# Kernel optimization log

Hardware: AMD Instinct MI355X
Metric: run time of the kernel (lower is better)

## Reference

```python
import jax, jax.numpy as jnp
import numpy as np

B, S, D, H, E = 8, 196, 768, 12, 8
HD = D // H  # 64
FF = 4 * D   # 3072
EPS = 1e-5


def setup_inputs() -> dict:
    key = jax.random.key(0)
    ks = jax.random.split(key, 12)
    s = 0.02
    inp = {
        'x': jax.random.normal(ks[0], (B, S, D), jnp.float32),
        'ln1_g': jnp.ones((D,), jnp.float32),
        'ln1_b': jnp.zeros((D,), jnp.float32),
        'Wq': jax.random.normal(ks[1], (D, D), jnp.float32) * s,
        'bq': jnp.zeros((D,), jnp.float32),
        'Wk': jax.random.normal(ks[2], (D, HD), jnp.float32) * s,
        'bk': jnp.zeros((HD,), jnp.float32),
        'Wv': jax.random.normal(ks[3], (D, HD), jnp.float32) * s,
        'bv': jnp.zeros((HD,), jnp.float32),
        'ln2_g': jnp.ones((D,), jnp.float32),
        'ln2_b': jnp.zeros((D,), jnp.float32),
        'Wg': jax.random.normal(ks[4], (D, E), jnp.float32) * s,
        'bg': jnp.zeros((E,), jnp.float32),
        'W1': jax.random.normal(ks[5], (E, D, FF), jnp.float32) * s,
        'b1': jnp.zeros((E, FF), jnp.float32),
        'W2': jax.random.normal(ks[6], (E, FF, D), jnp.float32) * s,
        'b2': jnp.zeros((E, D), jnp.float32),
    }
    return inp


def _layernorm(x, g, b):
    mu = jnp.mean(x, axis=-1, keepdims=True)
    var = jnp.var(x, axis=-1, keepdims=True)
    return (x - mu) * jax.lax.rsqrt(var + EPS) * g + b


def _rotate_half(x):
    x1, x2 = jnp.split(x, 2, axis=-1)
    return jnp.concatenate((-x2, x1), axis=-1)


def _rope(seq_len):
    inv_freq = 1.0 / (10000.0 ** (jnp.arange(0, HD, 2, dtype=jnp.float32) / HD))
    freqs = jnp.arange(seq_len, dtype=jnp.float32)[:, None] * inv_freq[None, :]
    emb = jnp.concatenate((freqs, freqs), axis=-1)  # [S, HD]
    return emb[None, :, None, :]  # [1, S, 1, HD]


def _attention(x, Wq, bq, Wk, bk, Wv, bv):
    b, s, _ = x.shape
    q = (x @ Wq + bq).reshape(b, s, H, HD)
    k = (x @ Wk + bk).reshape(b, s, 1, HD)
    v = (x @ Wv + bv).reshape(b, s, 1, HD)
    k = jnp.broadcast_to(k, (b, s, H, HD))
    v = jnp.broadcast_to(v, (b, s, H, HD))
    pe = _rope(s)
    cos, sin = jnp.cos(pe), jnp.sin(pe)
    q = q * cos + _rotate_half(q) * sin
    k = k * cos + _rotate_half(k) * sin
    scale = HD ** -0.5
    # NOTE: faithful to source -- matmul over the last two dims of [b,s,h,d],
    # i.e. attention across HEADS, not sequence positions.
    attn = jnp.einsum('bshd,bsgd->bshg', q, k) * scale
    attn = jax.nn.softmax(attn, axis=-1)
    out = jnp.einsum('bshg,bsgd->bshd', attn, v)
    return out.reshape(b, s, H * HD)


def _moe(x, Wg, bg, W1, b1, W2, b2):
    b, s, d = x.shape
    xt = x.reshape(-1, d)  # [T, D]
    gates = jax.nn.softmax(xt @ Wg + bg, axis=-1)
    top1 = jnp.argmax(gates, axis=-1)  # topk(k=2)[:,0] == argmax
    out = jnp.zeros_like(xt)
    for e in range(E):  # small fixed expert count
        h = jax.nn.gelu(xt @ W1[e] + b1[e], approximate=False)
        y = h @ W2[e] + b2[e]
        out = jnp.where((top1 == e)[:, None], y, out)
    return out.reshape(b, s, d)


def reference(x, ln1_g, ln1_b, Wq, bq, Wk, bk, Wv, bv, ln2_g, ln2_b, Wg, bg, W1, b1, W2, b2):
    res = x
    h = _layernorm(x, ln1_g, ln1_b)
    h = _attention(h, Wq, bq, Wk, bk, Wv, bv)
    x = res + h
    res = x
    h = _layernorm(x, ln2_g, ln2_b)
    h = _moe(h, Wg, bg, W1, b1, W2, b2)
    return res + h
```

## Files before the change

### kernel.cpp

```cpp
#include <hip/hip_runtime.h>


typedef unsigned short u16;
typedef short bf16x8_t __attribute__((ext_vector_type(8)));
typedef short bf16x4_t __attribute__((ext_vector_type(4)));
typedef float f32x4_t  __attribute__((ext_vector_type(4)));

#define T_TOK 1568
#define DM 768
#define HD 64
#define FF 3072
#define NE 8

#define OFF_CNT   0
#define OFF_BUCK  256
#define OFF_V     (OFF_BUCK + NE*T_TOK*4)
#define OFF_H1    (OFF_V + T_TOK*HD*4)
#define OFF_H2    (OFF_H1 + T_TOK*DM*2)
#define OFF_HMID  (OFF_H2 + T_TOK*DM*2)

__device__ __forceinline__ float bf2f(u16 h) {
    unsigned u = ((unsigned)h) << 16;
    return __builtin_bit_cast(float, u);
}
__device__ __forceinline__ u16 f2bf(float f) {
    unsigned u = __builtin_bit_cast(unsigned, f);
    unsigned r = (u + 0x7FFFu + ((u >> 16) & 1u)) >> 16;
    return (u16)r;
}
__device__ __forceinline__ float gelu_f(float x) {
    return 0.5f * x * (1.0f + erff(x * 0.70710678118654752440f));
}

__global__ __launch_bounds__(256) void k_ln1(const float* __restrict__ x,
                                             const float* __restrict__ g,
                                             const float* __restrict__ b,
                                             u16* __restrict__ h1) {
    int t = blockIdx.x, tid = threadIdx.x;
    const float* xr = x + (size_t)t * DM;
    float v0 = xr[tid], v1 = xr[tid + 256], v2 = xr[tid + 512];
    float s = v0 + v1 + v2;
#pragma unroll
    for (int m = 1; m < 64; m <<= 1) s += __shfl_xor(s, m);
    __shared__ float wr1[4], wr2[4];
    int lane = tid & 63, w = tid >> 6;
    if (lane == 0) wr1[w] = s;
    __syncthreads();
    float mu = (wr1[0] + wr1[1] + wr1[2] + wr1[3]) * (1.0f / DM);
    float d0 = v0 - mu, d1 = v1 - mu, d2 = v2 - mu;
    float vs = d0 * d0 + d1 * d1 + d2 * d2;
#pragma unroll
    for (int m = 1; m < 64; m <<= 1) vs += __shfl_xor(vs, m);
    if (lane == 0) wr2[w] = vs;
    __syncthreads();
    float var = (wr2[0] + wr2[1] + wr2[2] + wr2[3]) * (1.0f / DM);
    float rs = rsqrtf(var + 1e-5f);
    u16* hr = h1 + (size_t)t * DM;
    hr[tid]       = f2bf(d0 * rs * g[tid]       + b[tid]);
    hr[tid + 256] = f2bf(d1 * rs * g[tid + 256] + b[tid + 256]);
    hr[tid + 512] = f2bf(d2 * rs * g[tid + 512] + b[tid + 512]);
}

__global__ __launch_bounds__(256) void k_vproj(const u16* __restrict__ h1,
                                               const float* __restrict__ Wv,
                                               const float* __restrict__ bv,
                                               float* __restrict__ vout) {
    __shared__ __align__(16) u16 h1s[8 * DM];
    __shared__ float ps[4 * 8 * 64];
    int tid = threadIdx.x, tb = blockIdx.x * 8;
#pragma unroll
    for (int j = 0; j < 3; j++) {
        int cid = tid + 256 * j;
        int row = cid / 96, c = cid % 96;
        *(bf16x8_t*)&h1s[row * DM + c * 8] =
            *(const bf16x8_t*)&h1[(size_t)(tb + row) * DM + c * 8];
    }
    __syncthreads();
    int j = tid & 63, w = tid >> 6;
    float acc[8];
#pragma unroll
    for (int tt = 0; tt < 8; tt++) acc[tt] = 0.0f;
    const float* wp = Wv + (size_t)(w * 192) * HD + j;
    for (int kk = 0; kk < 192; kk += 4) {
        float w0 = wp[(size_t)(kk + 0) * HD];
        float w1 = wp[(size_t)(kk + 1) * HD];
        float w2 = wp[(size_t)(kk + 2) * HD];
        float w3 = wp[(size_t)(kk + 3) * HD];
        int kb = w * 192 + kk;
#pragma unroll
        for (int tt = 0; tt < 8; tt++) {
            bf16x4_t hh = *(const bf16x4_t*)&h1s[tt * DM + kb];
            acc[tt] += bf2f((u16)hh[0]) * w0 + bf2f((u16)hh[1]) * w1 +
                       bf2f((u16)hh[2]) * w2 + bf2f((u16)hh[3]) * w3;
        }
    }
#pragma unroll
    for (int tt = 0; tt < 8; tt++) ps[(w * 8 + tt) * 64 + j] = acc[tt];
    __syncthreads();
    int tg = tid >> 6;
#pragma unroll
    for (int s2 = 0; s2 < 2; s2++) {
        int tt = tg * 2 + s2;
        float v = ps[tt * 64 + j] + ps[(8 + tt) * 64 + j] +
                  ps[(16 + tt) * 64 + j] + ps[(24 + tt) * 64 + j] + bv[j];
        vout[(size_t)(tb + tt) * HD + j] = v;
    }
}

__global__ __launch_bounds__(256) void k_x2ln2gate(
        const float* __restrict__ x, const float* __restrict__ vws,
        const float* __restrict__ g2, const float* __restrict__ b2g,
        const float* __restrict__ Wg, const float* __restrict__ bg,
        const float* __restrict__ b2moe,
        u16* __restrict__ h2, float* __restrict__ out,
        int* __restrict__ cnt, int* __restrict__ buck) {
    __shared__ float wgs[NE * DM];
    __shared__ float g2s[DM], b2s[DM];
    int tid = threadIdx.x, tb = blockIdx.x * 8;
    for (int idx = tid; idx < NE * DM; idx += 256) {
        int e = idx / DM, c = idx % DM;
        wgs[idx] = Wg[(size_t)c * NE + e];
    }
    for (int idx = tid; idx < DM; idx += 256) { g2s[idx] = g2[idx]; b2s[idx] = b2g[idx]; }
    __syncthreads();
    int lane = tid & 63, w = tid >> 6;
    for (int ttl = 0; ttl < 2; ttl++) {
        int t = tb + w * 2 + ttl;
        float vl = vws[(size_t)t * HD + lane];
        const float* xp = x + (size_t)t * DM;
        float xv[12];
        float s = 0.0f;
#pragma unroll
        for (int i = 0; i < 12; i++) {
            float q = xp[lane + 64 * i] + vl;
            xv[i] = q; s += q;
        }
#pragma unroll
        for (int m = 1; m < 64; m <<= 1) s += __shfl_xor(s, m);
        float mu = s * (1.0f / DM);
        float vs = 0.0f;
#pragma unroll
        for (int i = 0; i < 12; i++) { float d = xv[i] - mu; vs += d * d; }
#pragma unroll
        for (int m = 1; m < 64; m <<= 1) vs += __shfl_xor(vs, m);
        float rs = rsqrtf(vs * (1.0f / DM) + 1e-5f);
        float le[NE];
#pragma unroll
        for (int e = 0; e < NE; e++) le[e] = 0.0f;
        u16* h2p = h2 + (size_t)t * DM;
#pragma unroll
        for (int i = 0; i < 12; i++) {
            int c = lane + 64 * i;
            float h = (xv[i] - mu) * rs * g2s[c] + b2s[c];
            h2p[c] = f2bf(h);
#pragma unroll
            for (int e = 0; e < NE; e++) le[e] += h * wgs[e * DM + c];
        }
#pragma unroll
        for (int e = 0; e < NE; e++) {
#pragma unroll
            for (int m = 1; m < 64; m <<= 1) le[e] += __shfl_xor(le[e], m);
        }
        float best = le[0] + bg[0]; int be = 0;
#pragma unroll
        for (int e = 1; e < NE; e++) {
            float q = le[e] + bg[e];
            if (q > best) { best = q; be = e; }
        }
        if (lane == 0) {
            int pos = atomicAdd(&cnt[be], 1);
            buck[be * T_TOK + pos] = t;
        }
        float* op = out + (size_t)t * DM;
        const float* bp = b2moe + (size_t)be * DM;
#pragma unroll
        for (int i = 0; i < 12; i++) {
            int c = lane + 64 * i;
            op[c] = xv[i] + bp[c];
        }
    }
}

__global__ __launch_bounds__(256, 2) void k_moe_gemm1(
        const u16* __restrict__ h2, const float* __restrict__ W1,
        const float* __restrict__ b1, const int* __restrict__ cnt,
        const int* __restrict__ buck, u16* __restrict__ hmid) {
    int nt = blockIdx.x, e = blockIdx.y, mt = blockIdx.z;
    int cnte = cnt[e];
    int m0 = mt * 128;
    if (m0 >= cnte) return;
    int n0 = nt * 64;
    const float* W1e = W1 + (size_t)e * DM * FF;
    __shared__ __align__(16) u16 As[128 * 72];
    __shared__ __align__(16) u16 Bs[64 * 72];
    int tid = threadIdx.x, lane = tid & 63, wid = tid >> 6;

    int arow = tid >> 3, ac = tid & 7;
    int atok[4];
#pragma unroll
    for (int j = 0; j < 4; j++) {
        int i = m0 + arow + 32 * j;
        atok[j] = (i < cnte) ? buck[e * T_TOK + i] : -1;
    }
    int bn = tid & 63, bkg = tid >> 6;

    f32x4_t acc[2][4];
#pragma unroll
    for (int mi = 0; mi < 2; mi++)
#pragma unroll
        for (int ni = 0; ni < 4; ni++) acc[mi][ni] = (f32x4_t){0.f, 0.f, 0.f, 0.f};

    bf16x8_t a_pre[4];
    float b_pre[16];
#pragma unroll
    for (int j = 0; j < 4; j++) {
        bf16x8_t v = {0, 0, 0, 0, 0, 0, 0, 0};
        if (atok[j] >= 0) v = *(const bf16x8_t*)&h2[(size_t)atok[j] * DM + ac * 8];
        a_pre[j] = v;
    }
    {
        const float* bp = W1e + (size_t)(bkg * 16) * FF + n0 + bn;
#pragma unroll
        for (int kk = 0; kk < 16; kk++) b_pre[kk] = bp[(size_t)kk * FF];
    }

    const int NK = DM / 64;
    for (int kt = 0; kt < NK; kt++) {
        __syncthreads();
#pragma unroll
        for (int j = 0; j < 4; j++)
            *(bf16x8_t*)&As[(arow + 32 * j) * 72 + ac * 8] = a_pre[j];
        {
            bf16x8_t p0, p1;
#pragma unroll
            for (int kk = 0; kk < 8; kk++) {
                p0[kk] = (short)f2bf(b_pre[kk]);
                p1[kk] = (short)f2bf(b_pre[kk + 8]);
            }
            *(bf16x8_t*)&Bs[bn * 72 + bkg * 16] = p0;
            *(bf16x8_t*)&Bs[bn * 72 + bkg * 16 + 8] = p1;
        }
        __syncthreads();
        if (kt + 1 < NK) {
            int k0 = (kt + 1) * 64;
#pragma unroll
            for (int j = 0; j < 4; j++) {
                bf16x8_t v = {0, 0, 0, 0, 0, 0, 0, 0};
                if (atok[j] >= 0)
                    v = *(const bf16x8_t*)&h2[(size_t)atok[j] * DM + k0 + ac * 8];
                a_pre[j] = v;
            }
            const float* bp = W1e + (size_t)(k0 + bkg * 16) * FF + n0 + bn;
#pragma unroll
            for (int kk = 0; kk < 16; kk++) b_pre[kk] = bp[(size_t)kk * FF];
        }
        int lr = lane & 15, q = lane >> 4;
#pragma unroll
        for (int s = 0; s < 2; s++) {
            bf16x8_t af[2], bfr[4];
#pragma unroll
            for (int mi = 0; mi < 2; mi++)
                af[mi] = *(const bf16x8_t*)&As[(wid * 32 + mi * 16 + lr) * 72 + s * 32 + q * 8];
#pragma unroll
            for (int ni = 0; ni < 4; ni++)
                bfr[ni] = *(const bf16x8_t*)&Bs[(ni * 16 + lr) * 72 + s * 32 + q * 8];
#pragma unroll
            for (int mi = 0; mi < 2; mi++)
#pragma unroll
                for (int ni = 0; ni < 4; ni++)
                    acc[mi][ni] = __builtin_amdgcn_mfma_f32_16x16x32_bf16(
                        af[mi], bfr[ni], acc[mi][ni], 0, 0, 0);
        }
    }
    int lr = lane & 15, q = lane >> 4;
    float bias[4];
#pragma unroll
    for (int ni = 0; ni < 4; ni++) bias[ni] = b1[(size_t)e * FF + n0 + ni * 16 + lr];
#pragma unroll
    for (int mi = 0; mi < 2; mi++) {
#pragma unroll
        for (int r = 0; r < 4; r++) {
            int i = m0 + wid * 32 + mi * 16 + q * 4 + r;
            if (i < cnte) {
                int t = buck[e * T_TOK + i];
                size_t base = (size_t)t * FF + n0;
#pragma unroll
                for (int ni = 0; ni < 4; ni++) {
                    float vv = acc[mi][ni][r] + bias[ni];
                    hmid[base + ni * 16 + lr] = f2bf(gelu_f(vv));
                }
            }
        }
    }
}

__global__ __launch_bounds__(256, 2) void k_moe_gemm2(
        const u16* __restrict__ hmid, const float* __restrict__ W2,
        const int* __restrict__ cnt, const int* __restrict__ buck,
        float* __restrict__ out) {
    int nt = blockIdx.x, e = blockIdx.y, z = blockIdx.z;
    int kc = z & 3, mt = z >> 2;
    int cnte = cnt[e];
    int m0 = mt * 128;
    if (m0 >= cnte) return;
    int n0 = nt * 64;
    int kbase = kc * (FF / 4);
    const float* W2e = W2 + (size_t)e * FF * DM;
    __shared__ __align__(16) u16 As[128 * 72];
    __shared__ __align__(16) u16 Bs[64 * 72];
    int tid = threadIdx.x, lane = tid & 63, wid = tid >> 6;

    int arow = tid >> 3, ac = tid & 7;
    int atok[4];
#pragma unroll
    for (int j = 0; j < 4; j++) {
        int i = m0 + arow + 32 * j;
        atok[j] = (i < cnte) ? buck[e * T_TOK + i] : -1;
    }
    int bn = tid & 63, bkg = tid >> 6;

    f32x4_t acc[2][4];
#pragma unroll
    for (int mi = 0; mi < 2; mi++)
#pragma unroll
        for (int ni = 0; ni < 4; ni++) acc[mi][ni] = (f32x4_t){0.f, 0.f, 0.f, 0.f};

    bf16x8_t a_pre[4];
    float b_pre[16];
#pragma unroll
    for (int j = 0; j < 4; j++) {
        bf16x8_t v = {0, 0, 0, 0, 0, 0, 0, 0};
        if (atok[j] >= 0)
            v = *(const bf16x8_t*)&hmid[(size_t)atok[j] * FF + kbase + ac * 8];
        a_pre[j] = v;
    }
    {
        const float* bp = W2e + (size_t)(kbase + bkg * 16) * DM + n0 + bn;
#pragma unroll
        for (int kk = 0; kk < 16; kk++) b_pre[kk] = bp[(size_t)kk * DM];
    }

    const int NK = (FF / 4) / 64;
    for (int kt = 0; kt < NK; kt++) {
        __syncthreads();
#pragma unroll
        for (int j = 0; j < 4; j++)
            *(bf16x8_t*)&As[(arow + 32 * j) * 72 + ac * 8] = a_pre[j];
        {
            bf16x8_t p0, p1;
#pragma unroll
            for (int kk = 0; kk < 8; kk++) {
                p0[kk] = (short)f2bf(b_pre[kk]);
                p1[kk] = (short)f2bf(b_pre[kk + 8]);
            }
            *(bf16x8_t*)&Bs[bn * 72 + bkg * 16] = p0;
            *(bf16x8_t*)&Bs[bn * 72 + bkg * 16 + 8] = p1;
        }
        __syncthreads();
        if (kt + 1 < NK) {
            int k0 = kbase + (kt + 1) * 64;
#pragma unroll
            for (int j = 0; j < 4; j++) {
                bf16x8_t v = {0, 0, 0, 0, 0, 0, 0, 0};
                if (atok[j] >= 0)
                    v = *(const bf16x8_t*)&hmid[(size_t)atok[j] * FF + k0 + ac * 8];
                a_pre[j] = v;
            }
            const float* bp = W2e + (size_t)(k0 + bkg * 16) * DM + n0 + bn;
#pragma unroll
            for (int kk = 0; kk < 16; kk++) b_pre[kk] = bp[(size_t)kk * DM];
        }
        int lr = lane & 15, q = lane >> 4;
#pragma unroll
        for (int s = 0; s < 2; s++) {
            bf16x8_t af[2], bfr[4];
#pragma unroll
            for (int mi = 0; mi < 2; mi++)
                af[mi] = *(const bf16x8_t*)&As[(wid * 32 + mi * 16 + lr) * 72 + s * 32 + q * 8];
#pragma unroll
            for (int ni = 0; ni < 4; ni++)
                bfr[ni] = *(const bf16x8_t*)&Bs[(ni * 16 + lr) * 72 + s * 32 + q * 8];
#pragma unroll
            for (int mi = 0; mi < 2; mi++)
#pragma unroll
                for (int ni = 0; ni < 4; ni++)
                    acc[mi][ni] = __builtin_amdgcn_mfma_f32_16x16x32_bf16(
                        af[mi], bfr[ni], acc[mi][ni], 0, 0, 0);
        }
    }
    int lr = lane & 15, q = lane >> 4;
#pragma unroll
    for (int mi = 0; mi < 2; mi++) {
#pragma unroll
        for (int r = 0; r < 4; r++) {
            int i = m0 + wid * 32 + mi * 16 + q * 4 + r;
            if (i < cnte) {
                int t = buck[e * T_TOK + i];
                size_t base = (size_t)t * DM + n0;
#pragma unroll
                for (int ni = 0; ni < 4; ni++)
                    atomicAdd(&out[base + ni * 16 + lr], acc[mi][ni][r]);
            }
        }
    }
}

extern "C" void kernel_launch(void* const* d_in, const int* in_sizes, int n_in,
                              void* d_out, int out_size, void* d_ws, size_t ws_size,
                              hipStream_t stream) {
    const float* x    = (const float*)d_in[0];
    const float* ln1g = (const float*)d_in[1];
    const float* ln1b = (const float*)d_in[2];
    const float* Wv   = (const float*)d_in[7];
    const float* bv   = (const float*)d_in[8];
    const float* ln2g = (const float*)d_in[9];
    const float* ln2b = (const float*)d_in[10];
    const float* Wg   = (const float*)d_in[11];
    const float* bg   = (const float*)d_in[12];
    const float* W1   = (const float*)d_in[13];
    const float* b1   = (const float*)d_in[14];
    const float* W2   = (const float*)d_in[15];
    const float* b2   = (const float*)d_in[16];

    char* ws = (char*)d_ws;
    int*   cnt  = (int*)(ws + OFF_CNT);
    int*   buck = (int*)(ws + OFF_BUCK);
    float* vws  = (float*)(ws + OFF_V);
    u16*   h1   = (u16*)(ws + OFF_H1);
    u16*   h2   = (u16*)(ws + OFF_H2);
    u16*   hmid = (u16*)(ws + OFF_HMID);
    float* out  = (float*)d_out;

    hipMemsetAsync(cnt, 0, NE * sizeof(int), stream);
    k_ln1<<<T_TOK, 256, 0, stream>>>(x, ln1g, ln1b, h1);
    k_vproj<<<T_TOK / 8, 256, 0, stream>>>(h1, Wv, bv, vws);
    k_x2ln2gate<<<T_TOK / 8, 256, 0, stream>>>(x, vws, ln2g, ln2b, Wg, bg, b2,
                                               h2, out, cnt, buck);
    k_moe_gemm1<<<dim3(FF / 64, NE, 13), 256, 0, stream>>>(h2, W1, b1, cnt, buck, hmid);
    k_moe_gemm2<<<dim3(DM / 64, NE, 52), 256, 0, stream>>>(hmid, W2, cnt, buck, out);
}
```

Before: 299.1 us.

## Fuse pre-MoE kernels and schedule expert GEMM tiles via compact work list

Merges LN1, the V projection and the residual/LN2/gate kernel into one kernel, so h1 and v stay in shared memory instead of going through global memory and two launches are removed. Adds a single-thread planning kernel that builds a compact list of (expert, 64-row tile) work items. The expert GEMMs drop from 128-row to 64-row tiles and run as persistent grid-stride loops over that list, which avoids launching many empty blocks and improves load balance across uneven expert counts. The cost is an extra serial launch, smaller tiles with less weight reuse per block (W1/W2 are re-read and re-converted more often), and higher shared-memory use in the fused kernel.

```diff
diff --git a/kernel.cpp b/kernel.cpp
--- a/kernel.cpp
+++ b/kernel.cpp
@@ -13,11 +13,12 @@
 #define NE 8
 
 #define OFF_CNT   0
-#define OFF_BUCK  256
-#define OFF_V     (OFF_BUCK + NE*T_TOK*4)
-#define OFF_H1    (OFF_V + T_TOK*HD*4)
-#define OFF_H2    (OFF_H1 + T_TOK*DM*2)
-#define OFF_HMID  (OFF_H2 + T_TOK*DM*2)
+#define OFF_N12   32
+#define OFF_ITEM1 64
+#define OFF_ITEM2 864
+#define OFF_BUCK  4096
+#define OFF_H2    54272
+#define OFF_HMID  2462720
 
 __device__ __forceinline__ float bf2f(u16 h) {
     unsigned u = ((unsigned)h) << 16;
@@ -32,55 +33,59 @@
     return 0.5f * x * (1.0f + erff(x * 0.70710678118654752440f));
 }
 
-__global__ __launch_bounds__(256) void k_ln1(const float* __restrict__ x,
-                                             const float* __restrict__ g,
-                                             const float* __restrict__ b,
-                                             u16* __restrict__ h1) {
-    int t = blockIdx.x, tid = threadIdx.x;
-    const float* xr = x + (size_t)t * DM;
-    float v0 = xr[tid], v1 = xr[tid + 256], v2 = xr[tid + 512];
-    float s = v0 + v1 + v2;
-#pragma unroll
-    for (int m = 1; m < 64; m <<= 1) s += __shfl_xor(s, m);
-    __shared__ float wr1[4], wr2[4];
-    int lane = tid & 63, w = tid >> 6;
-    if (lane == 0) wr1[w] = s;
+__global__ __launch_bounds__(256) void k_pre(
+        const float* __restrict__ x,
+        const float* __restrict__ g1, const float* __restrict__ b1,
+        const float* __restrict__ Wv, const float* __restrict__ bv,
+        const float* __restrict__ g2, const float* __restrict__ b2g,
+        const float* __restrict__ Wg, const float* __restrict__ bg,
+        const float* __restrict__ b2moe,
+        u16* __restrict__ h2, float* __restrict__ out,
+        int* __restrict__ cnt, int* __restrict__ buck) {
+    __shared__ __align__(16) u16 h1s[8 * DM];
+    __shared__ float wgs[NE * DM];
+    __shared__ float g2s[DM], b2s[DM];
+    __shared__ float ps[4 * 8 * 64];
+    __shared__ float vsm[8 * 64];
+    int tid = threadIdx.x, lane = tid & 63, w = tid >> 6;
+    int tb = blockIdx.x * 8;
+
+    for (int idx = tid; idx < NE * DM; idx += 256) {
+        int e = idx / DM, c = idx % DM;
+        wgs[idx] = Wg[(size_t)c * NE + e];
+    }
+    for (int idx = tid; idx < DM; idx += 256) { g2s[idx] = g2[idx]; b2s[idx] = b2g[idx]; }
+
+    float xv[2][12];
+#pragma unroll
+    for (int ttl = 0; ttl < 2; ttl++) {
+        int tl = w * 2 + ttl;
+        int t = tb + tl;
+        const float* xp = x + (size_t)t * DM;
+        float s = 0.0f;
+#pragma unroll
+        for (int i = 0; i < 12; i++) { float q = xp[lane + 64 * i]; xv[ttl][i] = q; s += q; }
+#pragma unroll
+        for (int m = 1; m < 64; m <<= 1) s += __shfl_xor(s, m);
+        float mu = s * (1.0f / DM);
+        float vs = 0.0f;
+#pragma unroll
+        for (int i = 0; i < 12; i++) { float d = xv[ttl][i] - mu; vs += d * d; }
+#pragma unroll
+        for (int m = 1; m < 64; m <<= 1) vs += __shfl_xor(vs, m);
+        float rs = rsqrtf(vs * (1.0f / DM) + 1e-5f);
+#pragma unroll
+        for (int i = 0; i < 12; i++) {
+            int c = lane + 64 * i;
+            h1s[tl * DM + c] = f2bf((xv[ttl][i] - mu) * rs * g1[c] + b1[c]);
+        }
+    }
     __syncthreads();
-    float mu = (wr1[0] + wr1[1] + wr1[2] + wr1[3]) * (1.0f / DM);
-    float d0 = v0 - mu, d1 = v1 - mu, d2 = v2 - mu;
-    float vs = d0 * d0 + d1 * d1 + d2 * d2;
-#pragma unroll
-    for (int m = 1; m < 64; m <<= 1) vs += __shfl_xor(vs, m);
-    if (lane == 0) wr2[w] = vs;
-    __syncthreads();
-    float var = (wr2[0] + wr2[1] + wr2[2] + wr2[3]) * (1.0f / DM);
-    float rs = rsqrtf(var + 1e-5f);
-    u16* hr = h1 + (size_t)t * DM;
-    hr[tid]       = f2bf(d0 * rs * g[tid]       + b[tid]);
-    hr[tid + 256] = f2bf(d1 * rs * g[tid + 256] + b[tid + 256]);
-    hr[tid + 512] = f2bf(d2 * rs * g[tid + 512] + b[tid + 512]);
-}
-
-__global__ __launch_bounds__(256) void k_vproj(const u16* __restrict__ h1,
-                                               const float* __restrict__ Wv,
-                                               const float* __restrict__ bv,
-                                               float* __restrict__ vout) {
-    __shared__ __align__(16) u16 h1s[8 * DM];
-    __shared__ float ps[4 * 8 * 64];
-    int tid = threadIdx.x, tb = blockIdx.x * 8;
-#pragma unroll
-    for (int j = 0; j < 3; j++) {
-        int cid = tid + 256 * j;
-        int row = cid / 96, c = cid % 96;
-        *(bf16x8_t*)&h1s[row * DM + c * 8] =
-            *(const bf16x8_t*)&h1[(size_t)(tb + row) * DM + c * 8];
-    }
-    __syncthreads();
-    int j = tid & 63, w = tid >> 6;
+
     float acc[8];
 #pragma unroll
     for (int tt = 0; tt < 8; tt++) acc[tt] = 0.0f;
-    const float* wp = Wv + (size_t)(w * 192) * HD + j;
+    const float* wp = Wv + (size_t)(w * 192) * HD + lane;
     for (int kk = 0; kk < 192; kk += 4) {
         float w0 = wp[(size_t)(kk + 0) * HD];
         float w1 = wp[(size_t)(kk + 1) * HD];
@@ -95,52 +100,32 @@
         }
     }
 #pragma unroll
-    for (int tt = 0; tt < 8; tt++) ps[(w * 8 + tt) * 64 + j] = acc[tt];
+    for (int tt = 0; tt < 8; tt++) ps[(w * 8 + tt) * 64 + lane] = acc[tt];
     __syncthreads();
-    int tg = tid >> 6;
 #pragma unroll
     for (int s2 = 0; s2 < 2; s2++) {
-        int tt = tg * 2 + s2;
-        float v = ps[tt * 64 + j] + ps[(8 + tt) * 64 + j] +
-                  ps[(16 + tt) * 64 + j] + ps[(24 + tt) * 64 + j] + bv[j];
-        vout[(size_t)(tb + tt) * HD + j] = v;
-    }
-}
-
-__global__ __launch_bounds__(256) void k_x2ln2gate(
-        const float* __restrict__ x, const float* __restrict__ vws,
-        const float* __restrict__ g2, const float* __restrict__ b2g,
-        const float* __restrict__ Wg, const float* __restrict__ bg,
-        const float* __restrict__ b2moe,
-        u16* __restrict__ h2, float* __restrict__ out,
-        int* __restrict__ cnt, int* __restrict__ buck) {
-    __shared__ float wgs[NE * DM];
-    __shared__ float g2s[DM], b2s[DM];
-    int tid = threadIdx.x, tb = blockIdx.x * 8;
-    for (int idx = tid; idx < NE * DM; idx += 256) {
-        int e = idx / DM, c = idx % DM;
-        wgs[idx] = Wg[(size_t)c * NE + e];
-    }
-    for (int idx = tid; idx < DM; idx += 256) { g2s[idx] = g2[idx]; b2s[idx] = b2g[idx]; }
+        int tt = w * 2 + s2;
+        vsm[tt * 64 + lane] = ps[tt * 64 + lane] + ps[(8 + tt) * 64 + lane] +
+                              ps[(16 + tt) * 64 + lane] + ps[(24 + tt) * 64 + lane] +
+                              bv[lane];
+    }
     __syncthreads();
-    int lane = tid & 63, w = tid >> 6;
+
+#pragma unroll
     for (int ttl = 0; ttl < 2; ttl++) {
-        int t = tb + w * 2 + ttl;
-        float vl = vws[(size_t)t * HD + lane];
-        const float* xp = x + (size_t)t * DM;
-        float xv[12];
+        int tl = w * 2 + ttl;
+        int t = tb + tl;
+        float vl = vsm[tl * 64 + lane];
+        float x2v[12];
         float s = 0.0f;
 #pragma unroll
-        for (int i = 0; i < 12; i++) {
-            float q = xp[lane + 64 * i] + vl;
-            xv[i] = q; s += q;
-        }
+        for (int i = 0; i < 12; i++) { float q = xv[ttl][i] + vl; x2v[i] = q; s += q; }
 #pragma unroll
         for (int m = 1; m < 64; m <<= 1) s += __shfl_xor(s, m);
         float mu = s * (1.0f / DM);
         float vs = 0.0f;
 #pragma unroll
-        for (int i = 0; i < 12; i++) { float d = xv[i] - mu; vs += d * d; }
+        for (int i = 0; i < 12; i++) { float d = x2v[i] - mu; vs += d * d; }
 #pragma unroll
         for (int m = 1; m < 64; m <<= 1) vs += __shfl_xor(vs, m);
         float rs = rsqrtf(vs * (1.0f / DM) + 1e-5f);
@@ -151,7 +136,7 @@
 #pragma unroll
         for (int i = 0; i < 12; i++) {
             int c = lane + 64 * i;
-            float h = (xv[i] - mu) * rs * g2s[c] + b2s[c];
+            float h = (x2v[i] - mu) * rs * g2s[c] + b2s[c];
             h2p[c] = f2bf(h);
 #pragma unroll
             for (int e = 0; e < NE; e++) le[e] += h * wgs[e * DM + c];
@@ -176,230 +161,220 @@
 #pragma unroll
         for (int i = 0; i < 12; i++) {
             int c = lane + 64 * i;
-            op[c] = xv[i] + bp[c];
-        }
-    }
-}
-
-__global__ __launch_bounds__(256, 2) void k_moe_gemm1(
+            op[c] = x2v[i] + bp[c];
+        }
+    }
+}
+
+__global__ void k_plan(const int* __restrict__ cnt, int* __restrict__ n12,
+                       int* __restrict__ item1, int* __restrict__ item2) {
+    if (threadIdx.x == 0) {
+        int n1 = 0, n2 = 0;
+        for (int e = 0; e < NE; e++) {
+            int mts = (cnt[e] + 63) >> 6;
+            for (int mt = 0; mt < mts; mt++) {
+                int code = e * 64 + mt;
+                item1[n1++] = code;
+                for (int kc = 0; kc < 4; kc++) item2[n2++] = code * 4 + kc;
+            }
+        }
+        n12[0] = n1; n12[1] = n2;
+    }
+}
+
+__global__ __launch_bounds__(256) void k_moe_gemm1(
         const u16* __restrict__ h2, const float* __restrict__ W1,
         const float* __restrict__ b1, const int* __restrict__ cnt,
+        const int* __restrict__ n12, const int* __restrict__ item1,
         const int* __restrict__ buck, u16* __restrict__ hmid) {
-    int nt = blockIdx.x, e = blockIdx.y, mt = blockIdx.z;
-    int cnte = cnt[e];
-    int m0 = mt * 128;
-    if (m0 >= cnte) return;
-    int n0 = nt * 64;
-    const float* W1e = W1 + (size_t)e * DM * FF;
-    __shared__ __align__(16) u16 As[128 * 72];
+    int nt = blockIdx.x, n0 = nt * 64;
+    int n1 = n12[0];
+    int tid = threadIdx.x, lane = tid & 63, wid = tid >> 6;
+    int arow = tid >> 3, ac = tid & 7;
+    int bn = tid & 63, bkg = tid >> 6;
+    int lr = lane & 15, q = lane >> 4;
+    __shared__ __align__(16) u16 As[64 * 72];
     __shared__ __align__(16) u16 Bs[64 * 72];
-    int tid = threadIdx.x, lane = tid & 63, wid = tid >> 6;
-
-    int arow = tid >> 3, ac = tid & 7;
-    int atok[4];
-#pragma unroll
-    for (int j = 0; j < 4; j++) {
-        int i = m0 + arow + 32 * j;
-        atok[j] = (i < cnte) ? buck[e * T_TOK + i] : -1;
-    }
-    int bn = tid & 63, bkg = tid >> 6;
-
-    f32x4_t acc[2][4];
-#pragma unroll
-    for (int mi = 0; mi < 2; mi++)
-#pragma unroll
-        for (int ni = 0; ni < 4; ni++) acc[mi][ni] = (f32x4_t){0.f, 0.f, 0.f, 0.f};
-
-    bf16x8_t a_pre[4];
-    float b_pre[16];
-#pragma unroll
-    for (int j = 0; j < 4; j++) {
-        bf16x8_t v = {0, 0, 0, 0, 0, 0, 0, 0};
-        if (atok[j] >= 0) v = *(const bf16x8_t*)&h2[(size_t)atok[j] * DM + ac * 8];
-        a_pre[j] = v;
-    }
-    {
-        const float* bp = W1e + (size_t)(bkg * 16) * FF + n0 + bn;
-#pragma unroll
-        for (int kk = 0; kk < 16; kk++) b_pre[kk] = bp[(size_t)kk * FF];
-    }
-
-    const int NK = DM / 64;
-    for (int kt = 0; kt < NK; kt++) {
-        __syncthreads();
-#pragma unroll
-        for (int j = 0; j < 4; j++)
-            *(bf16x8_t*)&As[(arow + 32 * j) * 72 + ac * 8] = a_pre[j];
+
+    for (int it = blockIdx.y; it < n1; it += gridDim.y) {
+        int code = item1[it];
+        int e = code >> 6, mt = code & 63;
+        int cnte = cnt[e], m0 = mt * 64;
+        const float* W1e = W1 + (size_t)e * DM * FF;
+        int atok[2];
+#pragma unroll
+        for (int j = 0; j < 2; j++) {
+            int i = m0 + arow + 32 * j;
+            atok[j] = (i < cnte) ? buck[e * T_TOK + i] : -1;
+        }
+        f32x4_t acc[4];
+#pragma unroll
+        for (int ni = 0; ni < 4; ni++) acc[ni] = (f32x4_t){0.f, 0.f, 0.f, 0.f};
+
+        bf16x8_t a_pre[2];
+        float b_pre[16];
+#pragma unroll
+        for (int j = 0; j < 2; j++) {
+            bf16x8_t v = {0, 0, 0, 0, 0, 0, 0, 0};
+            if (atok[j] >= 0) v = *(const bf16x8_t*)&h2[(size_t)atok[j] * DM + ac * 8];
+            a_pre[j] = v;
+        }
         {
-            bf16x8_t p0, p1;
-#pragma unroll
-            for (int kk = 0; kk < 8; kk++) {
-                p0[kk] = (short)f2bf(b_pre[kk]);
-                p1[kk] = (short)f2bf(b_pre[kk + 8]);
-            }
-            *(bf16x8_t*)&Bs[bn * 72 + bkg * 16] = p0;
-            *(bf16x8_t*)&Bs[bn * 72 + bkg * 16 + 8] = p1;
-        }
-        __syncthreads();
-        if (kt + 1 < NK) {
-            int k0 = (kt + 1) * 64;
-#pragma unroll
-            for (int j = 0; j < 4; j++) {
-                bf16x8_t v = {0, 0, 0, 0, 0, 0, 0, 0};
-                if (atok[j] >= 0)
-                    v = *(const bf16x8_t*)&h2[(size_t)atok[j] * DM + k0 + ac * 8];
-                a_pre[j] = v;
-            }
-            const float* bp = W1e + (size_t)(k0 + bkg * 16) * FF + n0 + bn;
+            const float* bp = W1e + (size_t)(bkg * 16) * FF + n0 + bn;
 #pragma unroll
             for (int kk = 0; kk < 16; kk++) b_pre[kk] = bp[(size_t)kk * FF];
         }
-        int lr = lane & 15, q = lane >> 4;
-#pragma unroll
-        for (int s = 0; s < 2; s++) {
-            bf16x8_t af[2], bfr[4];
-#pragma unroll
-            for (int mi = 0; mi < 2; mi++)
-                af[mi] = *(const bf16x8_t*)&As[(wid * 32 + mi * 16 + lr) * 72 + s * 32 + q * 8];
-#pragma unroll
-            for (int ni = 0; ni < 4; ni++)
-                bfr[ni] = *(const bf16x8_t*)&Bs[(ni * 16 + lr) * 72 + s * 32 + q * 8];
-#pragma unroll
-            for (int mi = 0; mi < 2; mi++)
-#pragma unroll
-                for (int ni = 0; ni < 4; ni++)
-                    acc[mi][ni] = __builtin_amdgcn_mfma_f32_16x16x32_bf16(
-                        af[mi], bfr[ni], acc[mi][ni], 0, 0, 0);
-        }
-    }
-    int lr = lane & 15, q = lane >> 4;
-    float bias[4];
-#pragma unroll
-    for (int ni = 0; ni < 4; ni++) bias[ni] = b1[(size_t)e * FF + n0 + ni * 16 + lr];
-#pragma unroll
-    for (int mi = 0; mi < 2; mi++) {
+        const int NK = DM / 64;
+        for (int kt = 0; kt < NK; kt++) {
+            __syncthreads();
+#pragma unroll
+            for (int j = 0; j < 2; j++)
+                *(bf16x8_t*)&As[(arow + 32 * j) * 72 + ac * 8] = a_pre[j];
+            {
+                bf16x8_t p0, p1;
+#pragma unroll
+                for (int kk = 0; kk < 8; kk++) {
+                    p0[kk] = (short)f2bf(b_pre[kk]);
+                    p1[kk] = (short)f2bf(b_pre[kk + 8]);
+                }
+                *(bf16x8_t*)&Bs[bn * 72 + bkg * 16] = p0;
+                *(bf16x8_t*)&Bs[bn * 72 + bkg * 16 + 8] = p1;
+            }
+            __syncthreads();
+            if (kt + 1 < NK) {
+                int k0 = (kt + 1) * 64;
+#pragma unroll
+                for (int j = 0; j < 2; j++) {
+                    bf16x8_t v = {0, 0, 0, 0, 0, 0, 0, 0};
+                    if (atok[j] >= 0)
+                        v = *(const bf16x8_t*)&h2[(size_t)atok[j] * DM + k0 + ac * 8];
+                    a_pre[j] = v;
+                }
+                const float* bp = W1e + (size_t)(k0 + bkg * 16) * FF + n0 + bn;
+#pragma unroll
+                for (int kk = 0; kk < 16; kk++) b_pre[kk] = bp[(size_t)kk * FF];
+            }
+#pragma unroll
+            for (int s = 0; s < 2; s++) {
+                bf16x8_t af = *(const bf16x8_t*)&As[(wid * 16 + lr) * 72 + s * 32 + q * 8];
+#pragma unroll
+                for (int ni = 0; ni < 4; ni++) {
+                    bf16x8_t bfr = *(const bf16x8_t*)&Bs[(ni * 16 + lr) * 72 + s * 32 + q * 8];
+                    acc[ni] = __builtin_amdgcn_mfma_f32_16x16x32_bf16(af, bfr, acc[ni], 0, 0, 0);
+                }
+            }
+        }
+        float bias[4];
+#pragma unroll
+        for (int ni = 0; ni < 4; ni++) bias[ni] = b1[(size_t)e * FF + n0 + ni * 16 + lr];
 #pragma unroll
         for (int r = 0; r < 4; r++) {
-            int i = m0 + wid * 32 + mi * 16 + q * 4 + r;
+            int i = m0 + wid * 16 + q * 4 + r;
             if (i < cnte) {
                 int t = buck[e * T_TOK + i];
                 size_t base = (size_t)t * FF + n0;
 #pragma unroll
+                for (int ni = 0; ni < 4; ni++)
+                    hmid[base + ni * 16 + lr] = f2bf(gelu_f(acc[ni][r] + bias[ni]));
+            }
+        }
+    }
+}
+
+__global__ __launch_bounds__(256) void k_moe_gemm2(
+        const u16* __restrict__ hmid, const float* __restrict__ W2,
+        const int* __restrict__ cnt, const int* __restrict__ n12,
+        const int* __restrict__ item2, const int* __restrict__ buck,
+        float* __restrict__ out) {
+    int nt = blockIdx.x, n0 = nt * 64;
+    int n2 = n12[1];
+    int tid = threadIdx.x, lane = tid & 63, wid = tid >> 6;
+    int arow = tid >> 3, ac = tid & 7;
+    int bn = tid & 63, bkg = tid >> 6;
+    int lr = lane & 15, q = lane >> 4;
+    __shared__ __align__(16) u16 As[64 * 72];
+    __shared__ __align__(16) u16 Bs[64 * 72];
+
+    for (int it = blockIdx.y; it < n2; it += gridDim.y) {
+        int code2 = item2[it];
+        int kc = code2 & 3, code = code2 >> 2;
+        int e = code >> 6, mt = code & 63;
+        int cnte = cnt[e], m0 = mt * 64;
+        int kbase = kc * (FF / 4);
+        const float* W2e = W2 + (size_t)e * FF * DM;
+        int atok[2];
+#pragma unroll
+        for (int j = 0; j < 2; j++) {
+            int i = m0 + arow + 32 * j;
+            atok[j] = (i < cnte) ? buck[e * T_TOK + i] : -1;
+        }
+        f32x4_t acc[4];
+#pragma unroll
+        for (int ni = 0; ni < 4; ni++) acc[ni] = (f32x4_t){0.f, 0.f, 0.f, 0.f};
+
+        bf16x8_t a_pre[2];
+        float b_pre[16];
+#pragma unroll
+        for (int j = 0; j < 2; j++) {
+            bf16x8_t v = {0, 0, 0, 0, 0, 0, 0, 0};
+            if (atok[j] >= 0)
+                v = *(const bf16x8_t*)&hmid[(size_t)atok[j] * FF + kbase + ac * 8];
+            a_pre[j] = v;
+        }
+        {
+            const float* bp = W2e + (size_t)(kbase + bkg * 16) * DM + n0 + bn;
+#pragma unroll
+            for (int kk = 0; kk < 16; kk++) b_pre[kk] = bp[(size_t)kk * DM];
+        }
+        const int NK = (FF / 4) / 64;
+        for (int kt = 0; kt < NK; kt++) {
+            __syncthreads();
+#pragma unroll
+            for (int j = 0; j < 2; j++)
+                *(bf16x8_t*)&As[(arow + 32 * j) * 72 + ac * 8] = a_pre[j];
+            {
+                bf16x8_t p0, p1;
+#pragma unroll
+                for (int kk = 0; kk < 8; kk++) {
+                    p0[kk] = (short)f2bf(b_pre[kk]);
+                    p1[kk] = (short)f2bf(b_pre[kk + 8]);
+                }
+                *(bf16x8_t*)&Bs[bn * 72 + bkg * 16] = p0;
+                *(bf16x8_t*)&Bs[bn * 72 + bkg * 16 + 8] = p1;
+            }
+            __syncthreads();
+            if (kt + 1 < NK) {
+                int k0 = kbase + (kt + 1) * 64;
+#pragma unroll
+                for (int j = 0; j < 2; j++) {
+                    bf16x8_t v = {0, 0, 0, 0, 0, 0, 0, 0};
+                    if (atok[j] >= 0)
+                        v = *(const bf16x8_t*)&hmid[(size_t)atok[j] * FF + k0 + ac * 8];
+                    a_pre[j] = v;
+                }
+                const float* bp = W2e + (size_t)(k0 + bkg * 16) * DM + n0 + bn;
+#pragma unroll
+                for (int kk = 0; kk < 16; kk++) b_pre[kk] = bp[(size_t)kk * DM];
+            }
+#pragma unroll
+            for (int s = 0; s < 2; s++) {
+                bf16x8_t af = *(const bf16x8_t*)&As[(wid * 16 + lr) * 72 + s * 32 + q * 8];
+#pragma unroll
                 for (int ni = 0; ni < 4; ni++) {
-                    float vv = acc[mi][ni][r] + bias[ni];
-                    hmid[base + ni * 16 + lr] = f2bf(gelu_f(vv));
-                }
-            }
-        }
-    }
-}
-
-__global__ __launch_bounds__(256, 2) void k_moe_gemm2(
-        const u16* __restrict__ hmid, const float* __restrict__ W2,
-        const int* __restrict__ cnt, const int* __restrict__ buck,
-        float* __restrict__ out) {
-    int nt = blockIdx.x, e = blockIdx.y, z = blockIdx.z;
-    int kc = z & 3, mt = z >> 2;
-    int cnte = cnt[e];
-    int m0 = mt * 128;
-    if (m0 >= cnte) return;
-    int n0 = nt * 64;
-    int kbase = kc * (FF / 4);
-    const float* W2e = W2 + (size_t)e * FF * DM;
-    __shared__ __align__(16) u16 As[128 * 72];
-    __shared__ __align__(16) u16 Bs[64 * 72];
-    int tid = threadIdx.x, lane = tid & 63, wid = tid >> 6;
-
-    int arow = tid >> 3, ac = tid & 7;
-    int atok[4];
-#pragma unroll
-    for (int j = 0; j < 4; j++) {
-        int i = m0 + arow + 32 * j;
-        atok[j] = (i < cnte) ? buck[e * T_TOK + i] : -1;
-    }
-    int bn = tid & 63, bkg = tid >> 6;
-
-    f32x4_t acc[2][4];
-#pragma unroll
-    for (int mi = 0; mi < 2; mi++)
-#pragma unroll
-        for (int ni = 0; ni < 4; ni++) acc[mi][ni] = (f32x4_t){0.f, 0.f, 0.f, 0.f};
-
-    bf16x8_t a_pre[4];
-    float b_pre[16];
-#pragma unroll
-    for (int j = 0; j < 4; j++) {
-        bf16x8_t v = {0, 0, 0, 0, 0, 0, 0, 0};
-        if (atok[j] >= 0)
-            v = *(const bf16x8_t*)&hmid[(size_t)atok[j] * FF + kbase + ac * 8];
-        a_pre[j] = v;
-    }
-    {
-        const float* bp = W2e + (size_t)(kbase + bkg * 16) * DM + n0 + bn;
-#pragma unroll
-        for (int kk = 0; kk < 16; kk++) b_pre[kk] = bp[(size_t)kk * DM];
-    }
-
-    const int NK = (FF / 4) / 64;
-    for (int kt = 0; kt < NK; kt++) {
-        __syncthreads();
-#pragma unroll
-        for (int j = 0; j < 4; j++)
-            *(bf16x8_t*)&As[(arow + 32 * j) * 72 + ac * 8] = a_pre[j];
-        {
-            bf16x8_t p0, p1;
-#pragma unroll
-            for (int kk = 0; kk < 8; kk++) {
-                p0[kk] = (short)f2bf(b_pre[kk]);
-                p1[kk] = (short)f2bf(b_pre[kk + 8]);
-            }
-            *(bf16x8_t*)&Bs[bn * 72 + bkg * 16] = p0;
-            *(bf16x8_t*)&Bs[bn * 72 + bkg * 16 + 8] = p1;
-        }
-        __syncthreads();
-        if (kt + 1 < NK) {
-            int k0 = kbase + (kt + 1) * 64;
-#pragma unroll
-            for (int j = 0; j < 4; j++) {
-                bf16x8_t v = {0, 0, 0, 0, 0, 0, 0, 0};
-                if (atok[j] >= 0)
-                    v = *(const bf16x8_t*)&hmid[(size_t)atok[j] * FF + k0 + ac * 8];
-                a_pre[j] = v;
-            }
-            const float* bp = W2e + (size_t)(k0 + bkg * 16) * DM + n0 + bn;
-#pragma unroll
-            for (int kk = 0; kk < 16; kk++) b_pre[kk] = bp[(size_t)kk * DM];
-        }
-        int lr = lane & 15, q = lane >> 4;
-#pragma unroll
-        for (int s = 0; s < 2; s++) {
-            bf16x8_t af[2], bfr[4];
-#pragma unroll
-            for (int mi = 0; mi < 2; mi++)
-                af[mi] = *(const bf16x8_t*)&As[(wid * 32 + mi * 16 + lr) * 72 + s * 32 + q * 8];
-#pragma unroll
-            for (int ni = 0; ni < 4; ni++)
-                bfr[ni] = *(const bf16x8_t*)&Bs[(ni * 16 + lr) * 72 + s * 32 + q * 8];
-#pragma unroll
-            for (int mi = 0; mi < 2; mi++)
-#pragma unroll
-                for (int ni = 0; ni < 4; ni++)
-                    acc[mi][ni] = __builtin_amdgcn_mfma_f32_16x16x32_bf16(
-                        af[mi], bfr[ni], acc[mi][ni], 0, 0, 0);
-        }
-    }
-    int lr = lane & 15, q = lane >> 4;
-#pragma unroll
-    for (int mi = 0; mi < 2; mi++) {
+                    bf16x8_t bfr = *(const bf16x8_t*)&Bs[(ni * 16 + lr) * 72 + s * 32 + q * 8];
+                    acc[ni] = __builtin_amdgcn_mfma_f32_16x16x32_bf16(af, bfr, acc[ni], 0, 0, 0);
+                }
+            }
+        }
 #pragma unroll
         for (int r = 0; r < 4; r++) {
-            int i = m0 + wid * 32 + mi * 16 + q * 4 + r;
+            int i = m0 + wid * 16 + q * 4 + r;
             if (i < cnte) {
                 int t = buck[e * T_TOK + i];
                 size_t base = (size_t)t * DM + n0;
 #pragma unroll
                 for (int ni = 0; ni < 4; ni++)
-                    atomicAdd(&out[base + ni * 16 + lr], acc[mi][ni][r]);
+                    atomicAdd(&out[base + ni * 16 + lr], acc[ni][r]);
             }
         }
     }
@@ -423,19 +398,21 @@
     const float* b2   = (const float*)d_in[16];
 
     char* ws = (char*)d_ws;
-    int*   cnt  = (int*)(ws + OFF_CNT);
-    int*   buck = (int*)(ws + OFF_BUCK);
-    float* vws  = (float*)(ws + OFF_V);
-    u16*   h1   = (u16*)(ws + OFF_H1);
-    u16*   h2   = (u16*)(ws + OFF_H2);
-    u16*   hmid = (u16*)(ws + OFF_HMID);
-    float* out  = (float*)d_out;
-
-    hipMemsetAsync(cnt, 0, NE * sizeof(int), stream);
-    k_ln1<<<T_TOK, 256, 0, stream>>>(x, ln1g, ln1b, h1);
-    k_vproj<<<T_TOK / 8, 256, 0, stream>>>(h1, Wv, bv, vws);
-    k_x2ln2gate<<<T_TOK / 8, 256, 0, stream>>>(x, vws, ln2g, ln2b, Wg, bg, b2,
-                                               h2, out, cnt, buck);
-    k_moe_gemm1<<<dim3(FF / 64, NE, 13), 256, 0, stream>>>(h2, W1, b1, cnt, buck, hmid);
-    k_moe_gemm2<<<dim3(DM / 64, NE, 52), 256, 0, stream>>>(hmid, W2, cnt, buck, out);
-}
+    int*   cnt   = (int*)(ws + OFF_CNT);
+    int*   n12   = (int*)(ws + OFF_N12);
+    int*   item1 = (int*)(ws + OFF_ITEM1);
+    int*   item2 = (int*)(ws + OFF_ITEM2);
+    int*   buck  = (int*)(ws + OFF_BUCK);
+    u16*   h2    = (u16*)(ws + OFF_H2);
+    u16*   hmid  = (u16*)(ws + OFF_HMID);
+    float* out   = (float*)d_out;
+
+    hipMemsetAsync(cnt, 0, 16 * sizeof(int), stream);
+    k_pre<<<T_TOK / 8, 256, 0, stream>>>(x, ln1g, ln1b, Wv, bv, ln2g, ln2b,
+                                         Wg, bg, b2, h2, out, cnt, buck);
+    k_plan<<<1, 64, 0, stream>>>(cnt, n12, item1, item2);
+    k_moe_gemm1<<<dim3(FF / 64, 32), 256, 0, stream>>>(h2, W1, b1, cnt, n12,
+                                                       item1, buck, hmid);
+    k_moe_gemm2<<<dim3(DM / 64, 128), 256, 0, stream>>>(hmid, W2, cnt, n12,
+                                                        item2, buck, out);
+}
```

Result: slower. 321.8 us (+7.6%).
